# Performance work log

Hardware: AMD Instinct MI355X
Metric: run time of the kernel (lower is better)

Reference implementation:

```python
import jax, jax.numpy as jnp
import numpy as np

U = 2048
D = 2048
N_HEADS = 16
D_HEAD = D // N_HEADS
FFN_MULT = 4
D_FF = FFN_MULT * D
EPS = 1e-6


def _rmsnorm(x, w):
    # x: [U, D], w: [D]
    ms = jnp.mean(jnp.square(x), axis=-1, keepdims=True)
    return x * jax.lax.rsqrt(ms + EPS) * w


def setup_inputs() -> dict:
    key = jax.random.key(0)
    ks = jax.random.split(key, 12)
    d = {}
    d["x"] = jax.random.normal(ks[0], (U, D), dtype=jnp.float32)
    d["adj_bias"] = jax.random.normal(ks[1], (U, U), dtype=jnp.float32)
    # learned params (torch nn.Linear stores weight as [out, in]; y = x @ W.T)
    init = lambda k, shape, std: jax.random.normal(k, shape, dtype=jnp.float32) * std
    d["norm1_w"] = jnp.ones((D,), dtype=jnp.float32)
    d["norm2_w"] = jnp.ones((D,), dtype=jnp.float32)
    d["wq"] = init(ks[2], (D, D), (1.0 / D) ** 0.5)
    d["wk"] = init(ks[3], (D, D), (1.0 / D) ** 0.5)
    d["wv"] = init(ks[4], (D, D), (1.0 / D) ** 0.5)
    d["wo"] = init(ks[5], (D, D), (2.0 / D) ** 0.5)  # nn.init.normal_ std=(2/D)^0.5
    d["w_up"] = init(ks[6], (D_FF, D), (1.0 / D) ** 0.5)
    d["b_up"] = jnp.zeros((D_FF,), dtype=jnp.float32)
    d["w_down"] = init(ks[7], (D, D_FF), (2.0 / D_FF) ** 0.5)
    d["b_down"] = jnp.zeros((D,), dtype=jnp.float32)
    return d


def reference(x, adj_bias, norm1_w, norm2_w, wq, wk, wv, wo, w_up, b_up, w_down, b_down):
    scale = 1.0 / (D_HEAD ** 0.5)
    h = _rmsnorm(x, norm1_w)
    # project and split heads: [U, D] -> [H, U, d]
    q = (h @ wq.T).reshape(U, N_HEADS, D_HEAD).transpose(1, 0, 2)
    k = (h @ wk.T).reshape(U, N_HEADS, D_HEAD).transpose(1, 0, 2)
    v = (h @ wv.T).reshape(U, N_HEADS, D_HEAD).transpose(1, 0, 2)
    scores = jnp.einsum('hud,hvd->huv', q, k) * scale + adj_bias[None, :, :]
    attn = jax.nn.softmax(scores, axis=-1)
    out = jnp.einsum('huv,hvd->hud', attn, v)  # [H, U, d]
    out = out.transpose(1, 0, 2).reshape(U, D)
    x = x + out @ wo.T
    h2 = _rmsnorm(x, norm2_w)
    ff = jax.nn.gelu(h2 @ w_up.T + b_up, approximate=False)
    x = x + ff @ w_down.T + b_down
    return x
```

## Files before the change

kernel.cpp:

```cpp
#include <hip/hip_runtime.h>
#include <hip/hip_fp16.h>
#include <cstdint>
#include <cstddef>

#define U_DIM 2048
#define D_DIM 2048
#define NH 16
#define DH 128
#define DFF 8192
#define EPS_RMS 1e-6f
#define ATTN_SCALE 0.088388347648318447f

typedef unsigned short u16;
typedef __attribute__((ext_vector_type(4))) float floatx4;
typedef __attribute__((ext_vector_type(8))) short shortx8;

__device__ __forceinline__ float bf2f(u16 u) {
  union { unsigned int i; float f; } v; v.i = ((unsigned int)u) << 16; return v.f;
}
__device__ __forceinline__ u16 f2bf(float f) {
  union { float f; unsigned int i; } v; v.f = f;
  return (u16)((v.i + 0x7fffu + ((v.i >> 16) & 1u)) >> 16);
}
__device__ __forceinline__ u16 f2h(float f) {
  __half h = __float2half_rn(f);
  union { __half h; u16 u; } c; c.h = h; return c.u;
}
__device__ __forceinline__ float h2f(u16 u) {
  union { __half h; u16 u; } c; c.u = u; return __half2float(c.h);
}

__device__ __forceinline__ void f2b_body(const float* __restrict__ in,
                                         u16* __restrict__ out, int i, int n4) {
  if (i >= n4) return;
  float4 f = reinterpret_cast<const float4*>(in)[i];
  ushort4 o;
  o.x = f2bf(f.x); o.y = f2bf(f.y); o.z = f2bf(f.z); o.w = f2bf(f.w);
  reinterpret_cast<ushort4*>(out)[i] = o;
}

__global__ __launch_bounds__(256) void k_f2b4(
    const float* __restrict__ s0, const float* __restrict__ s1,
    const float* __restrict__ s2, const float* __restrict__ s3,
    u16* __restrict__ d0, u16* __restrict__ d1,
    u16* __restrict__ d2, u16* __restrict__ d3, int n4) {
  const float* s; u16* d;
  switch (blockIdx.y) {
    case 0: s = s0; d = d0; break;
    case 1: s = s1; d = d1; break;
    case 2: s = s2; d = d2; break;
    default: s = s3; d = d3; break;
  }
  f2b_body(s, d, blockIdx.x * 256 + threadIdx.x, n4);
}

__global__ __launch_bounds__(256) void k_f2b2(
    const float* __restrict__ s0, const float* __restrict__ s1,
    u16* __restrict__ d0, u16* __restrict__ d1, int n4) {
  const float* s = blockIdx.y ? s1 : s0;
  u16* d = blockIdx.y ? d1 : d0;
  f2b_body(s, d, blockIdx.x * 256 + threadIdx.x, n4);
}

__global__ __launch_bounds__(256) void k_prep_bias(const float* __restrict__ adj,
                                                   u16* __restrict__ adjp) {
  const int tile = blockIdx.x;
  const int qt = tile >> 4, kt = tile & 15;
  const int t = threadIdx.x;
  const int c16 = t & 15, rblk = t >> 4;
  u16* outt = adjp + (size_t)tile * 16384;
#pragma unroll
  for (int rr = 0; rr < 8; rr++) {
    int r = rblk * 8 + rr;
    const float* src = adj + (size_t)(qt * 128 + r) * U_DIM + kt * 128 + c16;
    ushort4 o0, o1;
    o0.x = f2h(src[0]);    o0.y = f2h(src[16]);  o0.z = f2h(src[32]);  o0.w = f2h(src[48]);
    o1.x = f2h(src[64]);   o1.y = f2h(src[80]);  o1.z = f2h(src[96]);  o1.w = f2h(src[112]);
    ushort4* dst = reinterpret_cast<ushort4*>(outt + ((size_t)c16 * 128 + r) * 8);
    dst[0] = o0; dst[1] = o1;
  }
}

__global__ __launch_bounds__(256) void k_reduce4(
    const u16* __restrict__ p0, const u16* __restrict__ p1,
    const u16* __restrict__ p2, const u16* __restrict__ p3,
    const float* __restrict__ X, const float* __restrict__ bias,
    float* __restrict__ out, int n4) {
  int i = blockIdx.x * 256 + threadIdx.x;
  if (i >= n4) return;
  ushort4 a = reinterpret_cast<const ushort4*>(p0)[i];
  ushort4 b = reinterpret_cast<const ushort4*>(p1)[i];
  ushort4 c = reinterpret_cast<const ushort4*>(p2)[i];
  ushort4 d = reinterpret_cast<const ushort4*>(p3)[i];
  float4 xv = reinterpret_cast<const float4*>(X)[i];
  float4 r;
  r.x = xv.x + bf2f(a.x) + bf2f(b.x) + bf2f(c.x) + bf2f(d.x);
  r.y = xv.y + bf2f(a.y) + bf2f(b.y) + bf2f(c.y) + bf2f(d.y);
  r.z = xv.z + bf2f(a.z) + bf2f(b.z) + bf2f(c.z) + bf2f(d.z);
  r.w = xv.w + bf2f(a.w) + bf2f(b.w) + bf2f(c.w) + bf2f(d.w);
  if (bias) {
    int col = (i * 4) & (D_DIM - 1);
    float4 bv = *reinterpret_cast<const float4*>(bias + col);
    r.x += bv.x; r.y += bv.y; r.z += bv.z; r.w += bv.w;
  }
  reinterpret_cast<float4*>(out)[i] = r;
}

__global__ __launch_bounds__(256) void k_reduce4norm(
    const u16* __restrict__ p0, const u16* __restrict__ p1,
    const u16* __restrict__ p2, const u16* __restrict__ p3,
    const float* __restrict__ X, const float* __restrict__ w,
    float* __restrict__ out, u16* __restrict__ nrm) {
  const int row = blockIdx.x;
  const int t = threadIdx.x;
  const size_t base = (size_t)row * 512;
  float4 r[2];
  float ss = 0.f;
#pragma unroll
  for (int h = 0; h < 2; h++) {
    size_t i = base + t + h * 256;
    ushort4 a = reinterpret_cast<const ushort4*>(p0)[i];
    ushort4 b = reinterpret_cast<const ushort4*>(p1)[i];
    ushort4 c = reinterpret_cast<const ushort4*>(p2)[i];
    ushort4 d = reinterpret_cast<const ushort4*>(p3)[i];
    float4 xv = reinterpret_cast<const float4*>(X)[i];
    float4 v;
    v.x = xv.x + bf2f(a.x) + bf2f(b.x) + bf2f(c.x) + bf2f(d.x);
    v.y = xv.y + bf2f(a.y) + bf2f(b.y) + bf2f(c.y) + bf2f(d.y);
    v.z = xv.z + bf2f(a.z) + bf2f(b.z) + bf2f(c.z) + bf2f(d.z);
    v.w = xv.w + bf2f(a.w) + bf2f(b.w) + bf2f(c.w) + bf2f(d.w);
    reinterpret_cast<float4*>(out)[i] = v;
    ss += v.x*v.x + v.y*v.y + v.z*v.z + v.w*v.w;
    r[h] = v;
  }
#pragma unroll
  for (int off = 32; off > 0; off >>= 1) ss += __shfl_xor(ss, off);
  __shared__ float red[4];
  if ((t & 63) == 0) red[t >> 6] = ss;
  __syncthreads();
  float tot = red[0] + red[1] + red[2] + red[3];
  float rms = rsqrtf(tot / (float)D_DIM + EPS_RMS);
  const float4* wr = reinterpret_cast<const float4*>(w);
#pragma unroll
  for (int h = 0; h < 2; h++) {
    float4 wv = wr[t + h * 256];
    ushort4 o;
    o.x = f2bf(r[h].x * rms * wv.x); o.y = f2bf(r[h].y * rms * wv.y);
    o.z = f2bf(r[h].z * rms * wv.z); o.w = f2bf(r[h].w * rms * wv.w);
    reinterpret_cast<ushort4*>(nrm)[base + t + h * 256] = o;
  }
}

__global__ __launch_bounds__(256) void k_rmsnorm(const float* __restrict__ x,
                                                 const float* __restrict__ w,
                                                 u16* __restrict__ out) {
  const int row = blockIdx.x;
  const int t = threadIdx.x;
  const float4* xr = reinterpret_cast<const float4*>(x + (size_t)row * D_DIM);
  float4 a0 = xr[t], a1 = xr[t + 256];
  float ss = a0.x*a0.x + a0.y*a0.y + a0.z*a0.z + a0.w*a0.w
           + a1.x*a1.x + a1.y*a1.y + a1.z*a1.z + a1.w*a1.w;
#pragma unroll
  for (int off = 32; off > 0; off >>= 1) ss += __shfl_xor(ss, off);
  __shared__ float red[4];
  if ((t & 63) == 0) red[t >> 6] = ss;
  __syncthreads();
  float tot = red[0] + red[1] + red[2] + red[3];
  float r = rsqrtf(tot / (float)D_DIM + EPS_RMS);
  const float4* wr = reinterpret_cast<const float4*>(w);
  float4 w0 = wr[t], w1 = wr[t + 256];
  ushort4 o0, o1;
  o0.x = f2bf(a0.x * r * w0.x); o0.y = f2bf(a0.y * r * w0.y);
  o0.z = f2bf(a0.z * r * w0.z); o0.w = f2bf(a0.w * r * w0.w);
  o1.x = f2bf(a1.x * r * w1.x); o1.y = f2bf(a1.y * r * w1.y);
  o1.z = f2bf(a1.z * r * w1.z); o1.w = f2bf(a1.w * r * w1.w);
  ushort4* op = reinterpret_cast<ushort4*>(out + (size_t)row * D_DIM);
  op[t] = o0; op[t + 256] = o1;
}

__device__ __forceinline__ void async16(u16* lds, const u16* g) {
  __builtin_amdgcn_global_load_lds(
      (__attribute__((address_space(1))) void*)(g),
      (__attribute__((address_space(3))) void*)(lds), 16, 0, 0);
}

#define BK64 64

__device__ __forceinline__ void gemm256_core(
    const u16* __restrict__ A, int lda,
    const u16* __restrict__ B, int ldb,
    int K, int bm, int bn, u16* smem, floatx4 acc[8][4]) {
  const int t = threadIdx.x;
  const int wv = t >> 6, lane = t & 63;
  const int wm = wv >> 2, wn = wv & 3;
  const int fr = lane & 15, kq = lane >> 4;
  const int srow = wv * 8 + (lane >> 3);
  const int scg  = (lane & 7) ^ (lane >> 3);
  const u16* Ag = A + (size_t)(bm + srow) * lda + scg * 8;
  const u16* Bg = B + (size_t)(bn + srow) * ldb + scg * 8;
  u16* AsW = smem + (wv * 8) * 64;
  u16* BsW = smem + 32768 + (wv * 8) * 64;
  const int swz  = fr & 7;
  const int arow = wm * 128 + fr;
  const int brow = wn * 64 + fr;
  const int nt = K / BK64;
#pragma unroll
  for (int r = 0; r < 4; r++) async16(AsW + r * 4096, Ag + (size_t)(r * 64) * lda);
#pragma unroll
  for (int r = 0; r < 4; r++) async16(BsW + r * 4096, Bg + (size_t)(r * 64) * ldb);
  int cur = 0;
  for (int kt = 0; kt < nt; kt++) {
    asm volatile("s_waitcnt vmcnt(0)" ::: "memory");
    __builtin_amdgcn_sched_barrier(0);
    __builtin_amdgcn_s_barrier();
    asm volatile("" ::: "memory");
    if (kt + 1 < nt) {
      const int nb = (cur ^ 1) * 16384;
      const size_t ko = (size_t)(kt + 1) * BK64;
#pragma unroll
      for (int r = 0; r < 4; r++) async16(AsW + nb + r * 4096, Ag + (size_t)(r * 64) * lda + ko);
#pragma unroll
      for (int r = 0; r < 4; r++) async16(BsW + nb + r * 4096, Bg + (size_t)(r * 64) * ldb + ko);
    }
    const u16* Ab = smem + cur * 16384;
    const u16* Bb = smem + 32768 + cur * 16384;
    shortx8 af[4], bf[4];
#pragma unroll
    for (int ph = 0; ph < 4; ph++) {
      const int ksub = ph >> 1;
      const int mh   = ph & 1;
      const int cswz = (((ksub * 4 + kq) ^ swz) * 8);
      if (mh == 0) {
#pragma unroll
        for (int i = 0; i < 4; i++)
          af[i] = *reinterpret_cast<const shortx8*>(Ab + (arow + i * 16) * 64 + cswz);
#pragma unroll
        for (int i = 0; i < 4; i++)
          bf[i] = *reinterpret_cast<const shortx8*>(Bb + (brow + i * 16) * 64 + cswz);
      } else {
#pragma unroll
        for (int i = 0; i < 4; i++)
          af[i] = *reinterpret_cast<const shortx8*>(Ab + (arow + (i + 4) * 16) * 64 + cswz);
      }
      asm volatile("s_waitcnt lgkmcnt(0)" ::: "memory");
      __builtin_amdgcn_sched_barrier(0);
      __builtin_amdgcn_s_setprio(1);
      const int m0 = mh * 4;
#pragma unroll
      for (int i = 0; i < 4; i++)
#pragma unroll
        for (int j = 0; j < 4; j++)
          acc[m0 + i][j] = __builtin_amdgcn_mfma_f32_16x16x32_bf16(af[i], bf[j], acc[m0 + i][j], 0, 0, 0);
      __builtin_amdgcn_s_setprio(0);
      if (ph < 3) { __builtin_amdgcn_s_barrier(); asm volatile("" ::: "memory"); }
    }
    cur ^= 1;
  }
}

#define GEMM256_PRELUDE                                           \
  __shared__ u16 smem[65536];                         \
  floatx4 acc[8][4];                                              \
  {                                                               \
    floatx4 zf = {0.f, 0.f, 0.f, 0.f};                            \
    for (int i = 0; i < 8; i++)                                   \
      for (int j = 0; j < 4; j++) acc[i][j] = zf;                 \
  }                                                               \
  const int bm = blockIdx.y * 256, bn = blockIdx.x * 256;

#define EPILOG256                                                 \
  const int lane_ = threadIdx.x & 63;                             \
  const int wv_ = threadIdx.x >> 6;                               \
  const int fr_ = lane_ & 15, kq_ = lane_ >> 4;                   \
  const int row0 = (wv_ >> 2) * 128 + kq_ * 4;                    \
  const int col0 = (wv_ & 3) * 64 + fr_;

__global__ __launch_bounds__(512, 1) void k_gemm_qkv(
    const u16* __restrict__ A, const u16* __restrict__ B,
    u16* __restrict__ Q, u16* __restrict__ Ko, u16* __restrict__ VT) {
  GEMM256_PRELUDE;
  gemm256_core(A, D_DIM, B, D_DIM, D_DIM, bm, bn, smem, acc);
  EPILOG256;
  if (bn < 4096) {
    u16* C = (bn < 2048) ? Q : Ko;
    const int cb = (bn < 2048) ? bn : bn - 2048;
#pragma unroll
    for (int mt = 0; mt < 8; mt++)
#pragma unroll
      for (int i = 0; i < 4; i++) {
        u16* cr = C + (size_t)(bm + row0 + mt*16 + i) * D_DIM + cb + col0;
#pragma unroll
        for (int nt = 0; nt < 4; nt++) cr[nt*16] = f2bf(acc[mt][nt][i]);
      }
  } else {
    const int cb = bn - 4096;
#pragma unroll
    for (int mt = 0; mt < 8; mt++)
#pragma unroll
      for (int nt = 0; nt < 4; nt++) {
        int col = cb + col0 + nt*16;
        int row = bm + row0 + mt*16;
        ushort4 o;
        o.x = f2bf(acc[mt][nt][0]); o.y = f2bf(acc[mt][nt][1]);
        o.z = f2bf(acc[mt][nt][2]); o.w = f2bf(acc[mt][nt][3]);
        *reinterpret_cast<ushort4*>(VT + (size_t)col * U_DIM + row) = o;
      }
  }
}

__global__ __launch_bounds__(512, 1) void k_gemm_splitk_part(
    const u16* __restrict__ A, int lda, const u16* __restrict__ B, int ldb,
    int Kc, u16* __restrict__ P, size_t pstride, int ldc) {
  GEMM256_PRELUDE;
  const int koff = blockIdx.z * Kc;
  gemm256_core(A + koff, lda, B + koff, ldb, Kc, bm, bn, smem, acc);
  u16* Pz = P + (size_t)blockIdx.z * pstride;
  EPILOG256;
#pragma unroll
  for (int mt = 0; mt < 8; mt++)
#pragma unroll
    for (int i = 0; i < 4; i++) {
      u16* cr = Pz + (size_t)(bm + row0 + mt*16 + i) * ldc + bn + col0;
#pragma unroll
      for (int nt = 0; nt < 4; nt++) cr[nt*16] = f2bf(acc[mt][nt][i]);
    }
}

__device__ __forceinline__ float fast_gelu(float v) {
  float u = v * (0.79788456080286536f + 0.035677408136300125f * v * v);
  float tt = fminf(fmaxf(2.f * u, -40.f), 40.f);
  float e = __expf(tt);
  return 0.5f * v * (1.f + (e - 1.f) / (e + 1.f));
}

__global__ __launch_bounds__(512, 1) void k_gemm_gelu(
    const u16* __restrict__ A, int lda, const u16* __restrict__ B, int ldb,
    int K, const float* __restrict__ bias, u16* __restrict__ C, int ldc) {
  GEMM256_PRELUDE;
  gemm256_core(A, lda, B, ldb, K, bm, bn, smem, acc);
  EPILOG256;
#pragma unroll
  for (int mt = 0; mt < 8; mt++)
#pragma unroll
    for (int i = 0; i < 4; i++) {
      size_t off = (size_t)(bm + row0 + mt*16 + i) * ldc + bn + col0;
#pragma unroll
      for (int nt = 0; nt < 4; nt++) {
        float v = acc[mt][nt][i] + bias[bn + col0 + nt*16];
        C[off + nt*16] = f2bf(fast_gelu(v));
      }
    }
}

__global__ __launch_bounds__(256) void k_flash(
    const u16* __restrict__ Q, const u16* __restrict__ K,
    const u16* __restrict__ VT, const u16* __restrict__ ADJP,
    u16* __restrict__ O) {
  __shared__ u16 smem[36864];
  const int qt = blockIdx.x, gh = blockIdx.y;
  const int t = threadIdx.x, wv = t >> 6, lane = t & 63;
  const int fr = lane & 15, kq = lane >> 4;
  const int c4 = lane & 3, r4 = lane >> 2;

  const u16* gq = Q + (size_t)(qt * 64) * D_DIM + gh * DH;
  const u16* gk = K + gh * DH;
  const u16* gv = VT + (size_t)(gh * DH) * U_DIM;

#pragma unroll
  for (int it = 0; it < 4; it++) {
    int row = wv * 16 + it * 4 + kq;
    int cg = (fr + row) & 15;
    async16(smem + row * 128 + fr * 8, gq + (size_t)row * D_DIM + cg * 8);
  }
  __builtin_amdgcn_s_waitcnt(0);
  __syncthreads();
  shortx8 qf[4];
#pragma unroll
  for (int ks = 0; ks < 4; ks++) {
    int row = wv * 16 + fr;
    int slot = ((ks * 4 + kq) - row) & 15;
    qf[ks] = *reinterpret_cast<const shortx8*>(smem + row * 128 + slot * 8);
  }
  __syncthreads();

  floatx4 oacc[8];
  float lrow[4];
#pragma unroll
  for (int nt = 0; nt < 8; nt++) { floatx4 z = {0.f,0.f,0.f,0.f}; oacc[nt] = z; }
#pragma unroll
  for (int i = 0; i < 4; i++) lrow[i] = 0.f;

  {
    u16* Ks = smem; u16* Vs = smem + 16384;
#pragma unroll
    for (int it = 0; it < 4; it++) {
      int row = wv * 16 + it * 4 + kq;
      int cg = (fr + row) & 15;
      async16(Ks + row * 128 + fr * 8, gk + (size_t)row * D_DIM + cg * 8);
    }
#pragma unroll
    for (int sub = 0; sub < 2; sub++)
#pragma unroll
      for (int it = 0; it < 2; it++) {
        int row = wv * 32 + it * 16 + r4;
        int cg = (c4 + (row >> 1)) & 3;
        async16(Vs + sub * 4096 + row * 32 + c4 * 8,
                gv + (size_t)row * U_DIM + sub * 32 + cg * 8);
      }
  }

  u16* Pb = smem + 32768;
  for (int kt64 = 0; kt64 < 32; kt64++) {
    const int cur = kt64 & 1;
    u16* Ks = smem + cur * 8192;
    u16* Vs = smem + 16384 + cur * 8192;
    asm volatile("s_waitcnt vmcnt(0)" ::: "memory");
    __builtin_amdgcn_s_barrier();
    asm volatile("" ::: "memory");
    if (kt64 < 31) {
      u16* Kn = smem + (1 - cur) * 8192;
      u16* Vn = smem + 16384 + (1 - cur) * 8192;
      const u16* gkn = gk + (size_t)((kt64 + 1) * 64) * D_DIM;
      const u16* gvn = gv + (kt64 + 1) * 64;
#pragma unroll
      for (int it = 0; it < 4; it++) {
        int row = wv * 16 + it * 4 + kq;
        int cg = (fr + row) & 15;
        async16(Kn + row * 128 + fr * 8, gkn + (size_t)row * D_DIM + cg * 8);
      }
#pragma unroll
      for (int sub = 0; sub < 2; sub++)
#pragma unroll
        for (int it = 0; it < 2; it++) {
          int row = wv * 32 + it * 16 + r4;
          int cg = (c4 + (row >> 1)) & 3;
          async16(Vn + sub * 4096 + row * 32 + c4 * 8,
                  gvn + (size_t)row * U_DIM + sub * 32 + cg * 8);
        }
    }

    floatx4 sacc[4];
    { floatx4 z = {0.f,0.f,0.f,0.f}; sacc[0]=z; sacc[1]=z; sacc[2]=z; sacc[3]=z; }
#pragma unroll
    for (int ks = 0; ks < 4; ks++) {
      int slotA = ((ks * 4 + kq) - fr) & 15;
      int slotB = ((ks * 4 + kq) - (16 + fr)) & 15;
      shortx8 kf0 = *reinterpret_cast<const shortx8*>(Ks + fr * 128 + slotA * 8);
      shortx8 kf1 = *reinterpret_cast<const shortx8*>(Ks + (16 + fr) * 128 + slotB * 8);
      shortx8 kf2 = *reinterpret_cast<const shortx8*>(Ks + (32 + fr) * 128 + slotA * 8);
      shortx8 kf3 = *reinterpret_cast<const shortx8*>(Ks + (48 + fr) * 128 + slotB * 8);
      sacc[0] = __builtin_amdgcn_mfma_f32_16x16x32_bf16(qf[ks], kf0, sacc[0], 0, 0, 0);
      sacc[1] = __builtin_amdgcn_mfma_f32_16x16x32_bf16(qf[ks], kf1, sacc[1], 0, 0, 0);
      sacc[2] = __builtin_amdgcn_mfma_f32_16x16x32_bf16(qf[ks], kf2, sacc[2], 0, 0, 0);
      sacc[3] = __builtin_amdgcn_mfma_f32_16x16x32_bf16(qf[ks], kf3, sacc[3], 0, 0, 0);
    }

    const u16* bt = ADJP + ((size_t)(qt >> 1) * 16 + (kt64 >> 1)) * 16384 + (kt64 & 1) * 4;
#pragma unroll
    for (int i = 0; i < 4; i++) {
      int rl = wv * 16 + kq * 4 + i;
      int r128 = (qt & 1) * 64 + rl;
      ushort4 bh = *reinterpret_cast<const ushort4*>(bt + ((size_t)fr * 128 + r128) * 8);
      float s0 = sacc[0][i] * ATTN_SCALE + h2f(bh.x);
      float s1 = sacc[1][i] * ATTN_SCALE + h2f(bh.y);
      float s2 = sacc[2][i] * ATTN_SCALE + h2f(bh.z);
      float s3 = sacc[3][i] * ATTN_SCALE + h2f(bh.w);
      float p0 = __expf(fminf(s0, 80.f));
      float p1 = __expf(fminf(s1, 80.f));
      float p2 = __expf(fminf(s2, 80.f));
      float p3 = __expf(fminf(s3, 80.f));
      int slot0 = ((fr >> 3) - (rl >> 1)) & 3;
      int slot1 = (((16 + fr) >> 3) - (rl >> 1)) & 3;
      Pb[rl * 64 + slot0 * 8 + (fr & 7)] = f2bf(p0);
      Pb[rl * 64 + slot1 * 8 + (fr & 7)] = f2bf(p1);
      Pb[rl * 64 + 32 + slot0 * 8 + (fr & 7)] = f2bf(p2);
      Pb[rl * 64 + 32 + slot1 * 8 + (fr & 7)] = f2bf(p3);
      lrow[i] += (p0 + p1) + (p2 + p3);
    }
    asm volatile("s_waitcnt lgkmcnt(0)" ::: "memory");
    __builtin_amdgcn_s_barrier();
    asm volatile("" ::: "memory");

    shortx8 pf0, pf1;
    {
      int row = wv * 16 + fr;
      int slot = (kq - (row >> 1)) & 3;
      pf0 = *reinterpret_cast<const shortx8*>(Pb + row * 64 + slot * 8);
      pf1 = *reinterpret_cast<const shortx8*>(Pb + row * 64 + 32 + slot * 8);
    }
#pragma unroll
    for (int nt = 0; nt < 8; nt++) {
      int row = nt * 16 + fr;
      int slot = (kq - (row >> 1)) & 3;
      shortx8 vf0 = *reinterpret_cast<const shortx8*>(Vs + row * 32 + slot * 8);
      shortx8 vf1 = *reinterpret_cast<const shortx8*>(Vs + 4096 + row * 32 + slot * 8);
      oacc[nt] = __builtin_amdgcn_mfma_f32_16x16x32_bf16(pf0, vf0, oacc[nt], 0, 0, 0);
      oacc[nt] = __builtin_amdgcn_mfma_f32_16x16x32_bf16(pf1, vf1, oacc[nt], 0, 0, 0);
    }
  }

#pragma unroll
  for (int i = 0; i < 4; i++) {
    int rl = wv * 16 + kq * 4 + i;
    float l = lrow[i];
    l += __shfl_xor(l, 1);
    l += __shfl_xor(l, 2);
    l += __shfl_xor(l, 4);
    l += __shfl_xor(l, 8);
    float inv = 1.f / l;
    u16* orow = O + (size_t)(qt * 64 + rl) * D_DIM + gh * DH + fr;
#pragma unroll
    for (int nt = 0; nt < 8; nt++)
      orow[nt * 16] = f2bf(oacc[nt][i] * inv);
  }
}

extern "C" void kernel_launch(void* const* d_in, const int* in_sizes, int n_in,
                              void* d_out, int out_size, void* d_ws, size_t ws_size,
                              hipStream_t stream) {
  (void)in_sizes; (void)n_in; (void)out_size; (void)ws_size;
  const float* x      = (const float*)d_in[0];
  const float* adj    = (const float*)d_in[1];
  const float* n1w    = (const float*)d_in[2];
  const float* n2w    = (const float*)d_in[3];
  const float* wq     = (const float*)d_in[4];
  const float* wk     = (const float*)d_in[5];
  const float* wv     = (const float*)d_in[6];
  const float* wo     = (const float*)d_in[7];
  const float* w_up   = (const float*)d_in[8];
  const float* b_up   = (const float*)d_in[9];
  const float* w_down = (const float*)d_in[10];
  const float* b_down = (const float*)d_in[11];
  float* out = (float*)d_out;
  char* ws = (char*)d_ws;
  const size_t MB = 1u << 20;
  u16* hb   = (u16*)(ws + 0*MB);
  u16* qb   = (u16*)(ws + 8*MB);
  u16* kb   = (u16*)(ws + 16*MB);
  u16* vtb  = (u16*)(ws + 24*MB);
  u16* adjp = (u16*)(ws + 32*MB);
  u16* aob  = (u16*)(ws + 40*MB);
  u16* wob  = (u16*)(ws + 48*MB);
  u16* wqkv = (u16*)(ws + 56*MB);
  u16* opp  = (u16*)(ws + 8*MB);
  u16* h2b  = (u16*)(ws + 0*MB);
  u16* wub  = (u16*)(ws + 8*MB);
  u16* ffb  = (u16*)(ws + 40*MB);
  u16* wdb  = (u16*)(ws + 72*MB);
  u16* dpp  = (u16*)(ws + 8*MB);

  dim3 blk(256);
  dim3 blk512(512);
  const int n4d = (D_DIM * D_DIM) / 4;
  const int n4f = (DFF * D_DIM) / 4;
  const size_t szd = (size_t)D_DIM * D_DIM;

  k_f2b4<<<dim3((n4d + 255) / 256, 4), blk, 0, stream>>>(
      wq, wk, wv, wo, wqkv, wqkv + szd, wqkv + 2*szd, wob, n4d);
  k_prep_bias<<<256, blk, 0, stream>>>(adj, adjp);
  k_rmsnorm<<<U_DIM, blk, 0, stream>>>(x, n1w, hb);

  k_gemm_qkv<<<dim3(24, 8), blk512, 0, stream>>>(hb, wqkv, qb, kb, vtb);

  k_flash<<<dim3(32, 16), blk, 0, stream>>>(qb, kb, vtb, adjp, aob);

  k_gemm_splitk_part<<<dim3(8, 8, 4), blk512, 0, stream>>>(
      aob, D_DIM, wob, D_DIM, D_DIM/4, opp, szd, D_DIM);
  k_reduce4norm<<<U_DIM, blk, 0, stream>>>(
      opp, opp + szd, opp + 2*szd, opp + 3*szd, x, n2w, out, h2b);

  k_f2b2<<<dim3((n4f + 255) / 256, 2), blk, 0, stream>>>(w_up, w_down, wub, wdb, n4f);
  k_gemm_gelu<<<dim3(32, 8), blk512, 0, stream>>>(h2b, D_DIM, wub, D_DIM, D_DIM,
                                                  b_up, ffb, DFF);
  k_gemm_splitk_part<<<dim3(8, 8, 4), blk512, 0, stream>>>(
      ffb, DFF, wdb, DFF, DFF/4, dpp, szd, D_DIM);
  k_reduce4<<<(n4d + 255) / 256, blk, 0, stream>>>(
      dpp, dpp + szd, dpp + 2*szd, dpp + 3*szd, out, b_down, out, n4d);
}
```

Baseline: 542.8 us.

## Use four-stage BK=32 LDS pipeline in 256x256 GEMM core

Replaces the double-buffered BK=64 K-loop with a four-slot ring of BK=32 half-tiles, prefetching three stages ahead and using graded vmcnt waits instead of draining all loads each iteration. The LDS swizzle and load mapping are reworked for the 32-element row width. This is meant to hide global load latency behind MFMA work. The cost is more barriers per unit of K and a new swizzle pattern that may produce more LDS bank conflicts.

```diff
diff --git a/kernel.cpp b/kernel.cpp
--- a/kernel.cpp
+++ b/kernel.cpp
@@ -184,7 +184,7 @@
       (__attribute__((address_space(3))) void*)(lds), 16, 0, 0);
 }
 
-#define BK64 64
+#define BKH 32
 
 __device__ __forceinline__ void gemm256_core(
     const u16* __restrict__ A, int lda,
@@ -194,67 +194,75 @@
   const int wv = t >> 6, lane = t & 63;
   const int wm = wv >> 2, wn = wv & 3;
   const int fr = lane & 15, kq = lane >> 4;
-  const int srow = wv * 8 + (lane >> 3);
-  const int scg  = (lane & 7) ^ (lane >> 3);
+  const int srow = wv * 16 + (lane >> 2);
+  const int scg  = (lane & 3) ^ ((lane >> 3) & 3);
   const u16* Ag = A + (size_t)(bm + srow) * lda + scg * 8;
   const u16* Bg = B + (size_t)(bn + srow) * ldb + scg * 8;
-  u16* AsW = smem + (wv * 8) * 64;
-  u16* BsW = smem + 32768 + (wv * 8) * 64;
-  const int swz  = fr & 7;
+  u16* AsW = smem + wv * 512;
+  u16* BsW = smem + 32768 + wv * 512;
+  const int ck   = (kq ^ ((fr >> 1) & 3)) * 8;
   const int arow = wm * 128 + fr;
   const int brow = wn * 64 + fr;
-  const int nt = K / BK64;
-#pragma unroll
-  for (int r = 0; r < 4; r++) async16(AsW + r * 4096, Ag + (size_t)(r * 64) * lda);
-#pragma unroll
-  for (int r = 0; r < 4; r++) async16(BsW + r * 4096, Bg + (size_t)(r * 64) * ldb);
-  int cur = 0;
-  for (int kt = 0; kt < nt; kt++) {
-    asm volatile("s_waitcnt vmcnt(0)" ::: "memory");
+  const int nh = K / BKH;
+#pragma unroll
+  for (int h0 = 0; h0 < 3; h0++) {
+    if (h0 < nh) {
+      const int hb = h0 * 8192;
+      const size_t ko = (size_t)h0 * BKH;
+      async16(AsW + hb,        Ag + ko);
+      async16(AsW + hb + 4096, Ag + (size_t)128 * lda + ko);
+      async16(BsW + hb,        Bg + ko);
+      async16(BsW + hb + 4096, Bg + (size_t)128 * ldb + ko);
+    }
+  }
+  for (int h = 0; h < nh; h++) {
+    const int rem = nh - 1 - h;
+    if (rem >= 2)      { asm volatile("s_waitcnt vmcnt(8)" ::: "memory"); }
+    else if (rem == 1) { asm volatile("s_waitcnt vmcnt(4)" ::: "memory"); }
+    else               { asm volatile("s_waitcnt vmcnt(0)" ::: "memory"); }
     __builtin_amdgcn_sched_barrier(0);
     __builtin_amdgcn_s_barrier();
     asm volatile("" ::: "memory");
-    if (kt + 1 < nt) {
-      const int nb = (cur ^ 1) * 16384;
-      const size_t ko = (size_t)(kt + 1) * BK64;
-#pragma unroll
-      for (int r = 0; r < 4; r++) async16(AsW + nb + r * 4096, Ag + (size_t)(r * 64) * lda + ko);
-#pragma unroll
-      for (int r = 0; r < 4; r++) async16(BsW + nb + r * 4096, Bg + (size_t)(r * 64) * ldb + ko);
-    }
-    const u16* Ab = smem + cur * 16384;
-    const u16* Bb = smem + 32768 + cur * 16384;
+    if (h + 3 < nh) {
+      const int hb = ((h + 3) & 3) * 8192;
+      const size_t ko = (size_t)(h + 3) * BKH;
+      async16(AsW + hb,        Ag + ko);
+      async16(AsW + hb + 4096, Ag + (size_t)128 * lda + ko);
+      async16(BsW + hb,        Bg + ko);
+      async16(BsW + hb + 4096, Bg + (size_t)128 * ldb + ko);
+    }
+    const u16* Ab = smem + (h & 3) * 8192;
+    const u16* Bb = smem + 32768 + (h & 3) * 8192;
     shortx8 af[4], bf[4];
 #pragma unroll
-    for (int ph = 0; ph < 4; ph++) {
-      const int ksub = ph >> 1;
-      const int mh   = ph & 1;
-      const int cswz = (((ksub * 4 + kq) ^ swz) * 8);
-      if (mh == 0) {
-#pragma unroll
-        for (int i = 0; i < 4; i++)
-          af[i] = *reinterpret_cast<const shortx8*>(Ab + (arow + i * 16) * 64 + cswz);
-#pragma unroll
-        for (int i = 0; i < 4; i++)
-          bf[i] = *reinterpret_cast<const shortx8*>(Bb + (brow + i * 16) * 64 + cswz);
-      } else {
-#pragma unroll
-        for (int i = 0; i < 4; i++)
-          af[i] = *reinterpret_cast<const shortx8*>(Ab + (arow + (i + 4) * 16) * 64 + cswz);
-      }
-      asm volatile("s_waitcnt lgkmcnt(0)" ::: "memory");
-      __builtin_amdgcn_sched_barrier(0);
-      __builtin_amdgcn_s_setprio(1);
-      const int m0 = mh * 4;
-#pragma unroll
-      for (int i = 0; i < 4; i++)
-#pragma unroll
-        for (int j = 0; j < 4; j++)
-          acc[m0 + i][j] = __builtin_amdgcn_mfma_f32_16x16x32_bf16(af[i], bf[j], acc[m0 + i][j], 0, 0, 0);
-      __builtin_amdgcn_s_setprio(0);
-      if (ph < 3) { __builtin_amdgcn_s_barrier(); asm volatile("" ::: "memory"); }
-    }
-    cur ^= 1;
+    for (int i = 0; i < 4; i++)
+      af[i] = *reinterpret_cast<const shortx8*>(Ab + (arow + i * 16) * 32 + ck);
+#pragma unroll
+    for (int i = 0; i < 4; i++)
+      bf[i] = *reinterpret_cast<const shortx8*>(Bb + (brow + i * 16) * 32 + ck);
+    asm volatile("s_waitcnt lgkmcnt(0)" ::: "memory");
+    __builtin_amdgcn_sched_barrier(0);
+    __builtin_amdgcn_s_setprio(1);
+#pragma unroll
+    for (int i = 0; i < 4; i++)
+#pragma unroll
+      for (int j = 0; j < 4; j++)
+        acc[i][j] = __builtin_amdgcn_mfma_f32_16x16x32_bf16(af[i], bf[j], acc[i][j], 0, 0, 0);
+    __builtin_amdgcn_s_setprio(0);
+    __builtin_amdgcn_s_barrier();
+    asm volatile("" ::: "memory");
+#pragma unroll
+    for (int i = 0; i < 4; i++)
+      af[i] = *reinterpret_cast<const shortx8*>(Ab + (arow + (i + 4) * 16) * 32 + ck);
+    asm volatile("s_waitcnt lgkmcnt(0)" ::: "memory");
+    __builtin_amdgcn_sched_barrier(0);
+    __builtin_amdgcn_s_setprio(1);
+#pragma unroll
+    for (int i = 0; i < 4; i++)
+#pragma unroll
+      for (int j = 0; j < 4; j++)
+        acc[i + 4][j] = __builtin_amdgcn_mfma_f32_16x16x32_bf16(af[i], bf[j], acc[i + 4][j], 0, 0, 0);
+    __builtin_amdgcn_s_setprio(0);
   }
 }
 
```

After: 547.4 us. About the same (+0.9%).

## Drop per-phase barriers in GEMM main loop and let compiler interleave LDS loads with MFMA

Applied to the files above, without the earlier changes.

The 256x256 GEMM inner loop used to run four lock-step phases, each with an explicit lgkmcnt wait, a scheduling barrier, setprio toggles and a workgroup barrier. These are replaced by a plain two-step k loop that loads B fragments once per k-substep and streams A fragments one at a time into the MFMAs. The compiler is then free to overlap LDS reads with matrix ops, and only one barrier per k-tile remains. The cost is that wave-level phase coordination and the priority hints are gone, so LDS bank contention or scheduling quality now depend on the compiler.

```diff
diff --git a/kernel.cpp b/kernel.cpp
--- a/kernel.cpp
+++ b/kernel.cpp
@@ -210,9 +210,10 @@
   for (int r = 0; r < 4; r++) async16(BsW + r * 4096, Bg + (size_t)(r * 64) * ldb);
   int cur = 0;
   for (int kt = 0; kt < nt; kt++) {
-    asm volatile("s_waitcnt vmcnt(0)" ::: "memory");
+    asm volatile("s_waitcnt vmcnt(0) lgkmcnt(0)" ::: "memory");
     __builtin_amdgcn_sched_barrier(0);
     __builtin_amdgcn_s_barrier();
+    __builtin_amdgcn_sched_barrier(0);
     asm volatile("" ::: "memory");
     if (kt + 1 < nt) {
       const int nb = (cur ^ 1) * 16384;
@@ -224,35 +225,20 @@
     }
     const u16* Ab = smem + cur * 16384;
     const u16* Bb = smem + 32768 + cur * 16384;
-    shortx8 af[4], bf[4];
-#pragma unroll
-    for (int ph = 0; ph < 4; ph++) {
-      const int ksub = ph >> 1;
-      const int mh   = ph & 1;
+#pragma unroll
+    for (int ksub = 0; ksub < 2; ksub++) {
       const int cswz = (((ksub * 4 + kq) ^ swz) * 8);
-      if (mh == 0) {
-#pragma unroll
-        for (int i = 0; i < 4; i++)
-          af[i] = *reinterpret_cast<const shortx8*>(Ab + (arow + i * 16) * 64 + cswz);
-#pragma unroll
-        for (int i = 0; i < 4; i++)
-          bf[i] = *reinterpret_cast<const shortx8*>(Bb + (brow + i * 16) * 64 + cswz);
-      } else {
-#pragma unroll
-        for (int i = 0; i < 4; i++)
-          af[i] = *reinterpret_cast<const shortx8*>(Ab + (arow + (i + 4) * 16) * 64 + cswz);
+      shortx8 bfr[4];
+#pragma unroll
+      for (int j = 0; j < 4; j++)
+        bfr[j] = *reinterpret_cast<const shortx8*>(Bb + (brow + j * 16) * 64 + cswz);
+#pragma unroll
+      for (int mi = 0; mi < 8; mi++) {
+        shortx8 afr = *reinterpret_cast<const shortx8*>(Ab + (arow + mi * 16) * 64 + cswz);
+#pragma unroll
+        for (int j = 0; j < 4; j++)
+          acc[mi][j] = __builtin_amdgcn_mfma_f32_16x16x32_bf16(afr, bfr[j], acc[mi][j], 0, 0, 0);
       }
-      asm volatile("s_waitcnt lgkmcnt(0)" ::: "memory");
-      __builtin_amdgcn_sched_barrier(0);
-      __builtin_amdgcn_s_setprio(1);
-      const int m0 = mh * 4;
-#pragma unroll
-      for (int i = 0; i < 4; i++)
-#pragma unroll
-        for (int j = 0; j < 4; j++)
-          acc[m0 + i][j] = __builtin_amdgcn_mfma_f32_16x16x32_bf16(af[i], bf[j], acc[m0 + i][j], 0, 0, 0);
-      __builtin_amdgcn_s_setprio(0);
-      if (ph < 3) { __builtin_amdgcn_s_barrier(); asm volatile("" ::: "memory"); }
     }
     cur ^= 1;
   }
```

Result: no change. 532.7 us (-1.9%).
